# Performance work log

Measured on AMD Instinct MI355X. Metric: run time of the kernel, lower is better.

## Reference

```python
import jax, jax.numpy as jnp
import numpy as np
from jax import lax

SCALE = 2
K_UP = 5


def conv2d(x, w, pad):
    return lax.conv_general_dilated(
        x, w, window_strides=(1, 1), padding=[(pad, pad), (pad, pad)],
        dimension_numbers=("NCHW", "OIHW", "NCHW"))


def bn(x, gamma, beta, mean, var, eps=1e-5):
    # eval-mode batchnorm, per-channel (NCHW)
    inv = gamma / jnp.sqrt(var + eps)
    return x * inv[None, :, None, None] + (beta - mean * inv)[None, :, None, None]


def pixel_shuffle(x, r):
    b, crr, h, w = x.shape
    c = crr // (r * r)
    x = x.reshape(b, c, r, r, h, w)
    x = x.transpose(0, 1, 4, 2, 5, 3)  # b, c, h, r, w, r
    return x.reshape(b, c, h * r, w * r)


def setup_inputs():
    key = jax.random.key(0)
    k0, k1, k2 = jax.random.split(key, 3)
    b, c, h, w = 2, 256, 64, 64
    cmid, cenc = 64, (SCALE * K_UP) ** 2  # 64, 100
    return {
        "X": jax.random.normal(k0, (b, c, h, w), jnp.float32),
        "comp_w": jax.random.normal(k1, (cmid, c, 1, 1), jnp.float32) * 0.05,
        "comp_gamma": jnp.ones((cmid,), jnp.float32),
        "comp_beta": jnp.zeros((cmid,), jnp.float32),
        "comp_mean": jnp.zeros((cmid,), jnp.float32),
        "comp_var": jnp.ones((cmid,), jnp.float32),
        "enc_w": jax.random.normal(k2, (cenc, cmid, 3, 3), jnp.float32) * 0.05,
        "enc_gamma": jnp.ones((cenc,), jnp.float32),
        "enc_beta": jnp.zeros((cenc,), jnp.float32),
        "enc_mean": jnp.zeros((cenc,), jnp.float32),
        "enc_var": jnp.ones((cenc,), jnp.float32),
        "power_p": jnp.ones((1,), jnp.float32),
    }


def reference(X, comp_w, comp_gamma, comp_beta, comp_mean, comp_var,
              enc_w, enc_gamma, enc_beta, enc_mean, enc_var, power_p):
    b, c, h, w = X.shape
    h_, w_ = h * SCALE, w * SCALE

    # kernel prediction branch
    W = conv2d(X, comp_w, 0)
    W = jax.nn.relu(bn(W, comp_gamma, comp_beta, comp_mean, comp_var))
    W = conv2d(W, enc_w, 1)
    W = bn(W, enc_gamma, enc_beta, enc_mean, enc_var)  # no relu
    W = pixel_shuffle(W, SCALE)  # (b, k_up^2, h_, w_)

    # power-normalized softmax: W = softmax(clamp(W)^clamp(p)) over taps
    i = jnp.clip(power_p, 1e-5)  # PowerIndex -> learnable scalar exponent
    W = jnp.clip(W, 1e-5)
    W = jnp.power(W, i[0])
    W = jax.nn.softmax(W, axis=1)

    # content branch: nearest upsample then dilated unfold (k=5, dil=2, pad=4)
    Xu = jnp.repeat(jnp.repeat(X, SCALE, axis=2), SCALE, axis=3)  # (b,c,h_,w_)
    pad = (K_UP // 2) * SCALE  # 4
    Xp = jnp.pad(Xu, ((0, 0), (0, 0), (pad, pad), (pad, pad)))
    patches = jnp.stack(
        [Xp[:, :, ki * SCALE: ki * SCALE + h_, kj * SCALE: kj * SCALE + w_]
         for ki in range(K_UP) for kj in range(K_UP)], axis=2)  # (b,c,25,h_,w_)

    return jnp.einsum("bkhw,bckhw->bchw", W, patches)
```

## Files before the change

kernel.cpp:

```cpp
#include <hip/hip_runtime.h>
#include <math.h>

#define NPX 4096
#define H2 128
#define W2 128
#define PP 66

__global__ __launch_bounds__(256) void k1_conv1x1(
    const float* __restrict__ X, const float* __restrict__ w,
    const float* __restrict__ g, const float* __restrict__ bt,
    const float* __restrict__ m, const float* __restrict__ var,
    float* __restrict__ mid_p)
{
    __shared__ float red[3 * 4 * 64];
    int tid = threadIdx.x;
    int x = tid & 63;
    int ciq = __builtin_amdgcn_readfirstlane(tid >> 6);
    int bx = blockIdx.x;
    int bb = bx >> 6, y = bx & 63;
    int co0 = blockIdx.y * 4;
    int ci0 = ciq * 64;

    const float* xp = X + ((size_t)(bb * 256 + ci0)) * NPX + y * 64 + x;
    const float* wp = w + (size_t)co0 * 256 + ci0;

    float acc[4] = {0.f, 0.f, 0.f, 0.f};

    #pragma unroll 8
    for (int ci = 0; ci < 64; ++ci) {
        float xv = xp[(size_t)ci * NPX];
        #pragma unroll
        for (int j = 0; j < 4; ++j)
            acc[j] += xv * wp[j * 256 + ci];
    }

    if (ciq > 0) {
        #pragma unroll
        for (int j = 0; j < 4; ++j)
            red[((ciq - 1) * 4 + j) * 64 + x] = acc[j];
    }
    __syncthreads();
    if (ciq == 0) {
        #pragma unroll
        for (int j = 0; j < 4; ++j) {
            float a = acc[j] + red[(0 * 4 + j) * 64 + x]
                             + red[(1 * 4 + j) * 64 + x]
                             + red[(2 * 4 + j) * 64 + x];
            int co = co0 + j;
            float inv = g[co] * rsqrtf(var[co] + 1e-5f);
            a = fmaxf(a * inv + (bt[co] - m[co] * inv), 0.f);
            mid_p[((size_t)(bb * 64 + co) * PP + (y + 1)) * PP + (x + 1)] = a;
        }
    }
}

__global__ __launch_bounds__(256) void k2a_conv3x3(
    const float* __restrict__ mid_p, const float* __restrict__ ew,
    float* __restrict__ enc)
{
    __shared__ float red[3 * 10 * 64];
    int tid = threadIdx.x;
    int x = tid & 63;
    int ciq = __builtin_amdgcn_readfirstlane(tid >> 6);
    int bx = blockIdx.x;
    int bb = bx >> 6, y = bx & 63;
    int co0 = blockIdx.y * 10;

    float acc[10];
    #pragma unroll
    for (int j = 0; j < 10; ++j) acc[j] = 0.f;

    const float* wb = ew + ((size_t)co0 * 64 + ciq * 16) * 9;

    #pragma unroll 2
    for (int ci = 0; ci < 16; ++ci) {
        const float* P = mid_p + (((size_t)(bb * 64 + ciq * 16 + ci)) * PP + y) * PP + x;
        float v0 = P[0],       v1 = P[1],          v2 = P[2];
        float v3 = P[PP],      v4 = P[PP + 1],     v5 = P[PP + 2];
        float v6 = P[2 * PP],  v7 = P[2 * PP + 1], v8 = P[2 * PP + 2];
        const float* wp = wb + ci * 9;
        #pragma unroll
        for (int j = 0; j < 10; ++j) {
            const float* wj = wp + j * 576;
            acc[j] += v0 * wj[0] + v1 * wj[1] + v2 * wj[2]
                    + v3 * wj[3] + v4 * wj[4] + v5 * wj[5]
                    + v6 * wj[6] + v7 * wj[7] + v8 * wj[8];
        }
    }

    if (ciq > 0) {
        #pragma unroll
        for (int j = 0; j < 10; ++j)
            red[((ciq - 1) * 10 + j) * 64 + x] = acc[j];
    }
    __syncthreads();
    if (ciq == 0) {
        #pragma unroll
        for (int j = 0; j < 10; ++j) {
            float a = acc[j] + red[(0 * 10 + j) * 64 + x]
                             + red[(1 * 10 + j) * 64 + x]
                             + red[(2 * 10 + j) * 64 + x];
            enc[((size_t)bb * 100 + co0 + j) * NPX + y * 64 + x] = a;
        }
    }
}

__global__ __launch_bounds__(64) void k2b_softmax(
    const float* __restrict__ enc,
    const float* __restrict__ g, const float* __restrict__ bt,
    const float* __restrict__ m, const float* __restrict__ var,
    const float* __restrict__ power_p,
    float* __restrict__ wn)
{
    int s = blockIdx.x & 3;
    int p = (blockIdx.x >> 2) * 64 + threadIdx.x;
    int bb = p >> 12, sp = p & (NPX - 1);
    float pw = fmaxf(power_p[0], 1e-5f);
    float tv[25];
    float mx = -1e30f;
    #pragma unroll
    for (int k = 0; k < 25; ++k) {
        int co = 4 * k + s;
        float inv = g[co] * rsqrtf(var[co] + 1e-5f);
        float e = enc[((size_t)bb * 100 + co) * NPX + sp] * inv + (bt[co] - m[co] * inv);
        e = fmaxf(e, 1e-5f);
        float xq = exp2f(pw * log2f(e));
        tv[k] = xq;
        mx = fmaxf(mx, xq);
    }
    float sum = 0.f;
    #pragma unroll
    for (int k = 0; k < 25; ++k) {
        float e = expf(tv[k] - mx);
        tv[k] = e;
        sum += e;
    }
    float r = 1.0f / sum;
    #pragma unroll
    for (int k = 0; k < 25; ++k)
        wn[((size_t)bb * 100 + s * 25 + k) * NPX + sp] = tv[k] * r;
}

__global__ __launch_bounds__(256) void k3_carafe(
    const float* __restrict__ X, const float* __restrict__ wn,
    float* __restrict__ out)
{
    __shared__ float xt[16 * 5 * 72];
    int tid = threadIdx.x;
    int px = tid & 63;
    int s = __builtin_amdgcn_readfirstlane(tid >> 6);
    int dy = s >> 1, dx = s & 1;
    int bx = blockIdx.x;
    int bb = bx >> 6, y = bx & 63;
    int c0 = blockIdx.y * 16;

    float wv[25];
    const float* wsrc = wn + ((size_t)bb * 100 + s * 25) * NPX + y * 64 + px;
    #pragma unroll
    for (int k = 0; k < 25; ++k)
        wv[k] = wsrc[(size_t)k * NPX];

    for (int idx = tid; idx < 5760; idx += 256) {
        int ch = idx / 360;
        int rem = idx - ch * 360;
        int r = rem / 72, c = rem - r * 72;
        int gy = y + r - 2, gx = c - 2;
        float val = 0.f;
        if (c < 68 && (unsigned)gy < 64u && (unsigned)gx < 64u)
            val = X[((size_t)(bb * 256 + c0 + ch)) * NPX + gy * 64 + gx];
        xt[idx] = val;
    }
    __syncthreads();

    int y2 = 2 * y + dy, x2 = 2 * px + dx;
    float* ob = out + ((size_t)(bb * 256 + c0) * H2 + y2) * W2 + x2;
    for (int ch = 0; ch < 16; ++ch) {
        const float* xb = &xt[ch * 360 + px];
        float a = 0.f;
        #pragma unroll
        for (int ki = 0; ki < 5; ++ki)
            #pragma unroll
            for (int kj = 0; kj < 5; ++kj)
                a += wv[ki * 5 + kj] * xb[ki * 72 + kj];
        ob[(size_t)ch * H2 * W2] = a;
    }
}

extern "C" void kernel_launch(void* const* d_in, const int* in_sizes, int n_in,
                              void* d_out, int out_size, void* d_ws, size_t ws_size,
                              hipStream_t stream)
{
    const float* X  = (const float*)d_in[0];
    const float* cw = (const float*)d_in[1];
    const float* cg = (const float*)d_in[2];
    const float* cb = (const float*)d_in[3];
    const float* cm = (const float*)d_in[4];
    const float* cv = (const float*)d_in[5];
    const float* ew = (const float*)d_in[6];
    const float* eg = (const float*)d_in[7];
    const float* eb = (const float*)d_in[8];
    const float* em = (const float*)d_in[9];
    const float* ev = (const float*)d_in[10];
    const float* pp = (const float*)d_in[11];
    float* out = (float*)d_out;

    float* ws   = (float*)d_ws;
    float* midp = ws;
    float* enc  = ws + 557568;
    float* wn   = ws + 557568 + 819200;

    hipMemsetAsync(midp, 0, 557568 * sizeof(float), stream);
    k1_conv1x1<<<dim3(128, 16), 256, 0, stream>>>(X, cw, cg, cb, cm, cv, midp);
    k2a_conv3x3<<<dim3(128, 10), 256, 0, stream>>>(midp, ew, enc);
    k2b_softmax<<<dim3(512), 64, 0, stream>>>(enc, eg, eb, em, ev, pp, wn);
    k3_carafe<<<dim3(128, 16), 256, 0, stream>>>(X, wn, out);
}
```

Measured before the change: 155.8 us.

## Widen conv1x1 output tile and remap CARAFE threads to channels with all sub-pixels

Measured after the change: 173.8 us. 11.6% more time.

```diff
diff --git a/kernel.cpp b/kernel.cpp
--- a/kernel.cpp
+++ b/kernel.cpp
@@ -12,40 +12,42 @@
     const float* __restrict__ m, const float* __restrict__ var,
     float* __restrict__ mid_p)
 {
-    __shared__ float red[3 * 4 * 64];
+    __shared__ float red[3 * 16 * 64];
     int tid = threadIdx.x;
     int x = tid & 63;
     int ciq = __builtin_amdgcn_readfirstlane(tid >> 6);
     int bx = blockIdx.x;
     int bb = bx >> 6, y = bx & 63;
-    int co0 = blockIdx.y * 4;
+    int co0 = blockIdx.y * 16;
     int ci0 = ciq * 64;
 
     const float* xp = X + ((size_t)(bb * 256 + ci0)) * NPX + y * 64 + x;
     const float* wp = w + (size_t)co0 * 256 + ci0;
 
-    float acc[4] = {0.f, 0.f, 0.f, 0.f};
+    float acc[16];
+    #pragma unroll
+    for (int j = 0; j < 16; ++j) acc[j] = 0.f;
 
     #pragma unroll 8
     for (int ci = 0; ci < 64; ++ci) {
         float xv = xp[(size_t)ci * NPX];
         #pragma unroll
-        for (int j = 0; j < 4; ++j)
+        for (int j = 0; j < 16; ++j)
             acc[j] += xv * wp[j * 256 + ci];
     }
 
     if (ciq > 0) {
         #pragma unroll
-        for (int j = 0; j < 4; ++j)
-            red[((ciq - 1) * 4 + j) * 64 + x] = acc[j];
+        for (int j = 0; j < 16; ++j)
+            red[((ciq - 1) * 16 + j) * 64 + x] = acc[j];
     }
     __syncthreads();
     if (ciq == 0) {
         #pragma unroll
-        for (int j = 0; j < 4; ++j) {
-            float a = acc[j] + red[(0 * 4 + j) * 64 + x]
-                             + red[(1 * 4 + j) * 64 + x]
-                             + red[(2 * 4 + j) * 64 + x];
+        for (int j = 0; j < 16; ++j) {
+            float a = acc[j] + red[(0 * 16 + j) * 64 + x]
+                             + red[(1 * 16 + j) * 64 + x]
+                             + red[(2 * 16 + j) * 64 + x];
             int co = co0 + j;
             float inv = g[co] * rsqrtf(var[co] + 1e-5f);
             a = fmaxf(a * inv + (bt[co] - m[co] * inv), 0.f);
@@ -148,17 +150,9 @@
     __shared__ float xt[16 * 5 * 72];
     int tid = threadIdx.x;
     int px = tid & 63;
-    int s = __builtin_amdgcn_readfirstlane(tid >> 6);
-    int dy = s >> 1, dx = s & 1;
     int bx = blockIdx.x;
     int bb = bx >> 6, y = bx & 63;
     int c0 = blockIdx.y * 16;
-
-    float wv[25];
-    const float* wsrc = wn + ((size_t)bb * 100 + s * 25) * NPX + y * 64 + px;
-    #pragma unroll
-    for (int k = 0; k < 25; ++k)
-        wv[k] = wsrc[(size_t)k * NPX];
 
     for (int idx = tid; idx < 5760; idx += 256) {
         int ch = idx / 360;
@@ -170,19 +164,35 @@
             val = X[((size_t)(bb * 256 + c0 + ch)) * NPX + gy * 64 + gx];
         xt[idx] = val;
     }
+
+    float wv[100];
+    const float* wsrc = wn + ((size_t)bb * 100) * NPX + y * 64 + px;
+    #pragma unroll
+    for (int t = 0; t < 100; ++t)
+        wv[t] = wsrc[(size_t)t * NPX];
+
     __syncthreads();
 
-    int y2 = 2 * y + dy, x2 = 2 * px + dx;
-    float* ob = out + ((size_t)(bb * 256 + c0) * H2 + y2) * W2 + x2;
-    for (int ch = 0; ch < 16; ++ch) {
+    int wq = __builtin_amdgcn_readfirstlane(tid >> 6);
+    #pragma unroll
+    for (int cc = 0; cc < 4; ++cc) {
+        int ch = wq * 4 + cc;
         const float* xb = &xt[ch * 360 + px];
-        float a = 0.f;
+        float a0 = 0.f, a1 = 0.f, a2 = 0.f, a3 = 0.f;
         #pragma unroll
         for (int ki = 0; ki < 5; ++ki)
             #pragma unroll
-            for (int kj = 0; kj < 5; ++kj)
-                a += wv[ki * 5 + kj] * xb[ki * 72 + kj];
-        ob[(size_t)ch * H2 * W2] = a;
+            for (int kj = 0; kj < 5; ++kj) {
+                float v = xb[ki * 72 + kj];
+                int k = ki * 5 + kj;
+                a0 += wv[k]      * v;
+                a1 += wv[25 + k] * v;
+                a2 += wv[50 + k] * v;
+                a3 += wv[75 + k] * v;
+            }
+        float* ob = out + ((size_t)(bb * 256 + c0 + ch) * H2 + 2 * y) * W2 + 2 * px;
+        ((float2*)ob)[0]        = make_float2(a0, a1);
+        ((float2*)(ob + W2))[0] = make_float2(a2, a3);
     }
 }
 
@@ -210,7 +220,7 @@
     float* wn   = ws + 557568 + 819200;
 
     hipMemsetAsync(midp, 0, 557568 * sizeof(float), stream);
-    k1_conv1x1<<<dim3(128, 16), 256, 0, stream>>>(X, cw, cg, cb, cm, cv, midp);
+    k1_conv1x1<<<dim3(128, 4), 256, 0, stream>>>(X, cw, cg, cb, cm, cv, midp);
     k2a_conv3x3<<<dim3(128, 10), 256, 0, stream>>>(midp, ew, enc);
     k2b_softmax<<<dim3(512), 64, 0, stream>>>(enc, eg, eb, em, ev, pp, wn);
     k3_carafe<<<dim3(128, 16), 256, 0, stream>>>(X, wn, out);
```

## Remap CARAFE warps to channel groups, reuse each LDS read across sub-pixels

Applied to the files above, without the earlier changes.

Result: no change. 153.2 us (-1.7%).

```diff
diff --git a/kernel.cpp b/kernel.cpp
--- a/kernel.cpp
+++ b/kernel.cpp
@@ -148,17 +148,9 @@
     __shared__ float xt[16 * 5 * 72];
     int tid = threadIdx.x;
     int px = tid & 63;
-    int s = __builtin_amdgcn_readfirstlane(tid >> 6);
-    int dy = s >> 1, dx = s & 1;
     int bx = blockIdx.x;
     int bb = bx >> 6, y = bx & 63;
     int c0 = blockIdx.y * 16;
-
-    float wv[25];
-    const float* wsrc = wn + ((size_t)bb * 100 + s * 25) * NPX + y * 64 + px;
-    #pragma unroll
-    for (int k = 0; k < 25; ++k)
-        wv[k] = wsrc[(size_t)k * NPX];
 
     for (int idx = tid; idx < 5760; idx += 256) {
         int ch = idx / 360;
@@ -172,17 +164,43 @@
     }
     __syncthreads();
 
-    int y2 = 2 * y + dy, x2 = 2 * px + dx;
-    float* ob = out + ((size_t)(bb * 256 + c0) * H2 + y2) * W2 + x2;
-    for (int ch = 0; ch < 16; ++ch) {
-        const float* xb = &xt[ch * 360 + px];
-        float a = 0.f;
-        #pragma unroll
-        for (int ki = 0; ki < 5; ++ki)
+    int wq = __builtin_amdgcn_readfirstlane(tid >> 6);
+
+    float a[4][4];
+    #pragma unroll
+    for (int i = 0; i < 4; ++i)
+        #pragma unroll
+        for (int j = 0; j < 4; ++j) a[i][j] = 0.f;
+
+    const float* wbase = wn + ((size_t)bb * 100) * NPX + y * 64 + px;
+    const float* xbase = xt + wq * 4 * 360 + px;
+
+    #pragma unroll 1
+    for (int ki = 0; ki < 5; ++ki) {
+        #pragma unroll
+        for (int kj = 0; kj < 5; ++kj) {
+            int k = ki * 5 + kj;
+            float w0 = wbase[(size_t)(k)      * NPX];
+            float w1 = wbase[(size_t)(25 + k) * NPX];
+            float w2 = wbase[(size_t)(50 + k) * NPX];
+            float w3 = wbase[(size_t)(75 + k) * NPX];
             #pragma unroll
-            for (int kj = 0; kj < 5; ++kj)
-                a += wv[ki * 5 + kj] * xb[ki * 72 + kj];
-        ob[(size_t)ch * H2 * W2] = a;
+            for (int cc = 0; cc < 4; ++cc) {
+                float v = xbase[cc * 360 + ki * 72 + kj];
+                a[cc][0] += w0 * v;
+                a[cc][1] += w1 * v;
+                a[cc][2] += w2 * v;
+                a[cc][3] += w3 * v;
+            }
+        }
+    }
+
+    #pragma unroll
+    for (int cc = 0; cc < 4; ++cc) {
+        int ch = wq * 4 + cc;
+        float* ob = out + ((size_t)(bb * 256 + c0 + ch) * H2 + 2 * y) * W2 + 2 * px;
+        ((float2*)ob)[0]        = make_float2(a[cc][0], a[cc][1]);
+        ((float2*)(ob + W2))[0] = make_float2(a[cc][2], a[cc][3]);
     }
 }
 
```
